# Kernel tuning notes

Measured on AMD Instinct MI355X. Metric: run time of the kernel, lower is better.

The kernel has to match this reference:

```python
import jax, jax.numpy as jnp
import numpy as np

B, U, C, M = 4096, 1024, 5000, 20

def setup_inputs() -> dict:
    key = jax.random.key(0)
    ks = jax.random.split(key, 9)
    inputs = jax.random.randint(ks[0], (B, 1), 0, C).astype(jnp.int32)
    states = 0.1 * jax.random.normal(ks[1], (B, U + 2), dtype=jnp.float32)
    bias_z = jnp.zeros((U,), jnp.float32)
    recurrent_kernel = 0.02 * jax.random.normal(ks[2], (U, 4 * U), dtype=jnp.float32)
    kernel_c = 0.02 * jax.random.normal(ks[3], (C, 4 * U), dtype=jnp.float32)
    bias = jnp.zeros((3 * U,), jnp.float32)
    kernel_d = 0.1 * jax.random.normal(ks[4], (2, 4 * U), dtype=jnp.float32)
    Wgmm_part1 = 0.05 * jax.random.normal(ks[5], (U, 3 * M), dtype=jnp.float32)
    bgmm_part1 = jnp.zeros((3 * M,), jnp.float32)
    return {"inputs": inputs, "states": states, "bias_z": bias_z,
            "recurrent_kernel": recurrent_kernel, "kernel_c": kernel_c,
            "bias": bias, "kernel_d": kernel_d,
            "Wgmm_part1": Wgmm_part1, "bgmm_part1": bgmm_part1}

def exp_safe(x):
    return jnp.clip(jnp.exp(x), 1e-10, 1e10)

def reference(inputs, states, bias_z, recurrent_kernel, kernel_c, bias,
              kernel_d, Wgmm_part1, bgmm_part1):
    u = bias_z.shape[0]
    h_tm1 = states[:, :-2]          # [B, U]
    _d = states[:, -2:]             # [B, 2]
    ch = inputs[:, 0].astype(jnp.int32)
    # one_hot(ch) @ kernel_c is just a row gather
    pre = kernel_c[ch] + _d @ kernel_d              # [B, 4U]
    # z and r gates share the left operand -> fuse into one matmul
    zr = (h_tm1 @ recurrent_kernel[:, :2 * u] + pre[:, :2 * u]
          + jnp.concatenate([bias_z, bias[:u]]))
    z = jax.nn.sigmoid(zr[:, :u])
    r = jax.nn.sigmoid(zr[:, u:])
    hh = jnp.tanh((r * h_tm1) @ recurrent_kernel[:, 2 * u:3 * u]
                  + pre[:, 2 * u:3 * u] + bias[u:2 * u])
    h = z * h_tm1 + (1.0 - z) * hh
    o = jnp.tanh(h @ recurrent_kernel[:, 3 * u:]
                 + pre[:, 3 * u:] + bias[2 * u:])
    gmm = o @ Wgmm_part1 + bgmm_part1               # [B, 3M]
    _pi, mux, muy = jnp.split(gmm, 3, axis=-1)
    e = exp_safe(_pi)
    pi = e / jnp.sum(e, axis=-1, keepdims=True)
    x_pred = jnp.sum(pi * mux, axis=-1, keepdims=True)
    y_pred = jnp.sum(pi * muy, axis=-1, keepdims=True)
    out = jnp.concatenate([o, pi, mux, muy, x_pred, y_pred], axis=-1)
    new_state = jnp.concatenate([h, x_pred, y_pred], axis=-1)
    return out, new_state
```

## Files before the change

### kernel.cpp

```cpp
#include <hip/hip_runtime.h>

typedef __attribute__((ext_vector_type(8))) short     bf16x8;
typedef __attribute__((ext_vector_type(4))) float     f32x4;
typedef __attribute__((ext_vector_type(2))) float     f32x2;
typedef __attribute__((ext_vector_type(4))) unsigned short u16x4;

#define OUT_STRIDE 1086
#define NS_STRIDE 1026
#define NS_BASE (4096*1086)

__device__ __forceinline__ unsigned short f2bf(float x) {
  unsigned int u = __float_as_uint(x);
  unsigned int r = (u + 0x7FFFu + ((u >> 16) & 1u)) >> 16;
  return (unsigned short)r;
}
__device__ __forceinline__ float bf2f(unsigned short u) {
  union { unsigned int i; float f; } v; v.i = ((unsigned int)u) << 16; return v.f;
}
__device__ __forceinline__ float sigmoidf(float x) { return 1.f / (1.f + expf(-x)); }

__device__ __forceinline__ void gld_lds16(const void* g, void* l) {
  __builtin_amdgcn_global_load_lds((const __attribute__((address_space(1))) void*)g,
                                   (__attribute__((address_space(3))) void*)l, 16, 0, 0);
}

__device__ __forceinline__ void decode_block(int bid, int& m0, int& n0) {
  const int swz = (bid & 7) * 64 + (bid >> 3);
  const int chunk = swz >> 6, l = swz & 63;
  m0 = ((chunk & 3) * 8 + (l >> 3)) * 128;
  n0 = ((chunk >> 2) * 8 + (l & 7)) * 64;
}

__global__ __launch_bounds__(256)
void transposeR(const float* __restrict__ R, unsigned short* __restrict__ Bt) {
  __shared__ float t[64][65];
  const int tx = threadIdx.x & 63, ty = threadIdx.x >> 6;
  const int j0 = blockIdx.x * 64, k0 = blockIdx.y * 64;
#pragma unroll
  for (int i = 0; i < 64; i += 4)
    t[ty + i][tx] = R[(size_t)(k0 + ty + i) * 4096 + j0 + tx];
  __syncthreads();
#pragma unroll
  for (int i = 0; i < 64; i += 4) {
    const int j = ty + i;
    Bt[(size_t)(j0 + j) * 1024 + k0 + tx] = f2bf(t[tx][j]);
  }
}

__global__ __launch_bounds__(256)
void convertH(const float* __restrict__ states, unsigned short* __restrict__ hb) {
  const int idx = blockIdx.x * 256 + threadIdx.x;
  const int b = idx >> 8, u = (idx & 255) * 4;
  const float* sp = states + (size_t)b * 1026 + u;
  f32x2 v0 = *(const f32x2*)sp, v1 = *(const f32x2*)(sp + 2);
  u16x4 w;
  w[0] = f2bf(v0[0]); w[1] = f2bf(v0[1]); w[2] = f2bf(v1[0]); w[3] = f2bf(v1[1]);
  *(u16x4*)&hb[(size_t)b * 1024 + u] = w;
}

__global__ __launch_bounds__(256)
void gemm_zr(const unsigned short* __restrict__ A,
             const unsigned short* __restrict__ Bt,
             const int* __restrict__ chv,
             const float* __restrict__ states,
             const float* __restrict__ kc,
             const float* __restrict__ kd,
             const float* __restrict__ bias_z,
             const float* __restrict__ bias,
             float* __restrict__ zbuf,
             unsigned short* __restrict__ rh) {
  __shared__ unsigned short Al[2][128 * 32];
  __shared__ unsigned short Bzl[2][64 * 32];
  __shared__ unsigned short Brl[2][64 * 32];
  __shared__ int   chs[128];
  __shared__ float d0s[128], d1s[128];

  const int tid = threadIdx.x, lane = tid & 63, wave = tid >> 6;
  int m0, n0;
  decode_block(blockIdx.x, m0, n0);

  if (tid < 128) {
    const int r = m0 + tid;
    chs[tid] = chv[r];
    d0s[tid] = states[(size_t)r * 1026 + 1024];
    d1s[tid] = states[(size_t)r * 1026 + 1025];
  }

  const unsigned short* Ag  = A  + (size_t)m0 * 1024;
  const unsigned short* Bzg = Bt + (size_t)n0 * 1024;
  const unsigned short* Brg = Bt + (size_t)(1024 + n0) * 1024;

  const int c1 = tid + 256;
  const int ar0 = tid >> 2, ak0 = (tid & 3) * 8;
  const int ar1 = c1 >> 2,  ak1 = (c1 & 3) * 8;

  f32x4 accz[2][4] = {}, accr[2][4] = {};

#define STAGE_ZR(b, kk)                                                        \
  gld_lds16(Ag  + (size_t)ar0 * 1024 + (kk) + ak0, &Al[b][tid * 8]);           \
  gld_lds16(Ag  + (size_t)ar1 * 1024 + (kk) + ak1, &Al[b][c1 * 8]);            \
  gld_lds16(Bzg + (size_t)ar0 * 1024 + (kk) + ak0, &Bzl[b][tid * 8]);          \
  gld_lds16(Brg + (size_t)ar0 * 1024 + (kk) + ak0, &Brl[b][tid * 8]);

  STAGE_ZR(0, 0);
  __syncthreads();

  const int arow = lane & 15, kg = (lane >> 4) * 8;
  for (int t = 0; t < 32; ++t) {
    const int cb = t & 1;
    if (t < 31) { STAGE_ZR(cb ^ 1, (t + 1) * 32); }
    bf16x8 af[2], bzf[4], brf[4];
#pragma unroll
    for (int mi = 0; mi < 2; ++mi)
      af[mi] = *(const bf16x8*)&Al[cb][(wave * 32 + mi * 16 + arow) * 32 + kg];
#pragma unroll
    for (int ni = 0; ni < 4; ++ni) {
      bzf[ni] = *(const bf16x8*)&Bzl[cb][(ni * 16 + arow) * 32 + kg];
      brf[ni] = *(const bf16x8*)&Brl[cb][(ni * 16 + arow) * 32 + kg];
    }
#pragma unroll
    for (int mi = 0; mi < 2; ++mi)
#pragma unroll
      for (int ni = 0; ni < 4; ++ni) {
        accz[mi][ni] = __builtin_amdgcn_mfma_f32_16x16x32_bf16(af[mi], bzf[ni], accz[mi][ni], 0, 0, 0);
        accr[mi][ni] = __builtin_amdgcn_mfma_f32_16x16x32_bf16(af[mi], brf[ni], accr[mi][ni], 0, 0, 0);
      }
    if (t < 31) __syncthreads();
  }
#undef STAGE_ZR

#pragma unroll
  for (int mi = 0; mi < 2; ++mi) {
#pragma unroll
    for (int r = 0; r < 4; ++r) {
      const int lrow = wave * 32 + mi * 16 + (lane >> 4) * 4 + r;
      const int grow = m0 + lrow;
      const int ch = chs[lrow];
      const float d0 = d0s[lrow], d1 = d1s[lrow];
      const float* kcrow = kc + (size_t)ch * 4096;
#pragma unroll
      for (int ni = 0; ni < 4; ++ni) {
        const int jc = n0 + ni * 16 + (lane & 15);
        const float vz = accz[mi][ni][r] + kcrow[jc]
                       + d0 * kd[jc] + d1 * kd[4096 + jc] + bias_z[jc];
        const float vr = accr[mi][ni][r] + kcrow[1024 + jc]
                       + d0 * kd[1024 + jc] + d1 * kd[4096 + 1024 + jc] + bias[jc];
        const float z = sigmoidf(vz);
        const float rr = sigmoidf(vr);
        zbuf[(size_t)grow * 1024 + jc] = z;
        rh[(size_t)grow * 1024 + jc] = f2bf(rr * bf2f(A[(size_t)grow * 1024 + jc]));
      }
    }
  }
}

template<int EPI>
__global__ __launch_bounds__(256)
void gemm_k(const unsigned short* __restrict__ A,
            const unsigned short* __restrict__ Bt,
            const int* __restrict__ chv,
            const float* __restrict__ states,
            const float* __restrict__ kc, int colbase,
            const float* __restrict__ kd,
            const float* __restrict__ bias, int biasoff,
            const float* __restrict__ zbuf,
            float* __restrict__ out2,
            unsigned short* __restrict__ hb2) {
  __shared__ unsigned short Al[2][128 * 32];
  __shared__ unsigned short Bl[2][64 * 32];
  __shared__ int   chs[128];
  __shared__ float d0s[128], d1s[128];

  const int tid = threadIdx.x, lane = tid & 63, wave = tid >> 6;
  int m0, n0;
  decode_block(blockIdx.x, m0, n0);

  if (tid < 128) {
    const int r = m0 + tid;
    chs[tid] = chv[r];
    d0s[tid] = states[(size_t)r * 1026 + 1024];
    d1s[tid] = states[(size_t)r * 1026 + 1025];
  }

  const unsigned short* Ag = A  + (size_t)m0 * 1024;
  const unsigned short* Bg = Bt + (size_t)n0 * 1024;

  const int c1 = tid + 256;
  const int ar0 = tid >> 2, ak0 = (tid & 3) * 8;
  const int ar1 = c1 >> 2,  ak1 = (c1 & 3) * 8;

  f32x4 acc[2][4] = {};

#define STAGE_K(b, kk)                                                         \
  gld_lds16(Ag + (size_t)ar0 * 1024 + (kk) + ak0, &Al[b][tid * 8]);            \
  gld_lds16(Ag + (size_t)ar1 * 1024 + (kk) + ak1, &Al[b][c1 * 8]);             \
  gld_lds16(Bg + (size_t)ar0 * 1024 + (kk) + ak0, &Bl[b][tid * 8]);

  STAGE_K(0, 0);
  __syncthreads();

  const int arow = lane & 15, kg = (lane >> 4) * 8;
  for (int t = 0; t < 32; ++t) {
    const int cb = t & 1;
    if (t < 31) { STAGE_K(cb ^ 1, (t + 1) * 32); }
    bf16x8 af[2], bf[4];
#pragma unroll
    for (int mi = 0; mi < 2; ++mi)
      af[mi] = *(const bf16x8*)&Al[cb][(wave * 32 + mi * 16 + arow) * 32 + kg];
#pragma unroll
    for (int ni = 0; ni < 4; ++ni)
      bf[ni] = *(const bf16x8*)&Bl[cb][(ni * 16 + arow) * 32 + kg];
#pragma unroll
    for (int mi = 0; mi < 2; ++mi)
#pragma unroll
      for (int ni = 0; ni < 4; ++ni)
        acc[mi][ni] = __builtin_amdgcn_mfma_f32_16x16x32_bf16(af[mi], bf[ni], acc[mi][ni], 0, 0, 0);
    if (t < 31) __syncthreads();
  }
#undef STAGE_K

#pragma unroll
  for (int mi = 0; mi < 2; ++mi) {
#pragma unroll
    for (int r = 0; r < 4; ++r) {
      const int lrow = wave * 32 + mi * 16 + (lane >> 4) * 4 + r;
      const int grow = m0 + lrow;
      const int ch = chs[lrow];
      const float d0 = d0s[lrow], d1 = d1s[lrow];
      const float* kcrow = kc + (size_t)ch * 4096 + colbase;
#pragma unroll
      for (int ni = 0; ni < 4; ++ni) {
        const int gcol = n0 + ni * 16 + (lane & 15);
        float v = acc[mi][ni][r] + kcrow[gcol]
                + d0 * kd[colbase + gcol] + d1 * kd[4096 + colbase + gcol]
                + bias[biasoff + gcol];
        if (EPI == 2) {
          const float hh = tanhf(v);
          const float z = zbuf[(size_t)grow * 1024 + gcol];
          const float htm = states[(size_t)grow * 1026 + gcol];
          const float h = z * htm + (1.f - z) * hh;
          out2[(size_t)grow * NS_STRIDE + gcol] = h;
          hb2[(size_t)grow * 1024 + gcol] = f2bf(h);
        } else {
          out2[(size_t)grow * OUT_STRIDE + gcol] = tanhf(v);
        }
      }
    }
  }
}

__global__ __launch_bounds__(512)
void gmm_kernel(const float* __restrict__ obuf,
                const float* __restrict__ Wg,
                const float* __restrict__ bg,
                float* __restrict__ outp,
                float* __restrict__ ns) {
  __shared__ float Wl[128 * 60 + 16];
  __shared__ float ol[8 * 1024];
  const int tid = threadIdx.x;
  const int lane = tid & 63;
  const int wave = tid >> 6;
  const int row0 = blockIdx.x * 8;

  for (int i = tid; i < 4096; i += 512) {
    const int rr = i >> 9, c2 = (i & 511) * 2;
    *(f32x2*)&ol[rr * 1024 + c2] = *(const f32x2*)&obuf[(size_t)(row0 + rr) * OUT_STRIDE + c2];
  }

  float g = 0.f;
  for (int kc0 = 0; kc0 < 1024; kc0 += 128) {
    __syncthreads();
    for (int i = tid; i < 1920; i += 512)
      *(f32x4*)&Wl[i * 4] = *(const f32x4*)&Wg[kc0 * 60 + i * 4];
    __syncthreads();
    const float* orow = &ol[wave * 1024 + kc0];
#pragma unroll 8
    for (int k = 0; k < 128; ++k)
      g = fmaf(orow[k], Wl[k * 60 + lane], g);
  }
  if (lane < 60) g += bg[lane];

  float e = 0.f;
  if (lane < 20) e = fminf(fmaxf(expf(g), 1e-10f), 1e10f);
  float s = e;
#pragma unroll
  for (int m = 1; m < 32; m <<= 1) s += __shfl_xor(s, m, 64);
  const float pi = (lane < 20) ? e / s : 0.f;
  const int src1 = (lane < 20) ? lane + 20 : lane;
  const int src2 = (lane < 20) ? lane + 40 : lane;
  const float mux = __shfl(g, src1, 64);
  const float muy = __shfl(g, src2, 64);
  float px = pi * mux, py = pi * muy;
#pragma unroll
  for (int m = 1; m < 32; m <<= 1) { px += __shfl_xor(px, m, 64); py += __shfl_xor(py, m, 64); }

  const int row = row0 + wave;
  float* orow = outp + (size_t)row * OUT_STRIDE;
  if (lane < 20) orow[1024 + lane] = pi;
  else if (lane < 60) orow[1024 + lane] = g;
  if (lane == 0) {
    orow[1084] = px;
    orow[1085] = py;
    ns[(size_t)row * NS_STRIDE + 1024] = px;
    ns[(size_t)row * NS_STRIDE + 1025] = py;
  }
}

extern "C" void kernel_launch(void* const* d_in, const int* in_sizes, int n_in,
                              void* d_out, int out_size, void* d_ws, size_t ws_size,
                              hipStream_t stream) {
  const int*   chv    = (const int*)d_in[0];
  const float* states = (const float*)d_in[1];
  const float* bias_z = (const float*)d_in[2];
  const float* R      = (const float*)d_in[3];
  const float* kc     = (const float*)d_in[4];
  const float* bias   = (const float*)d_in[5];
  const float* kd     = (const float*)d_in[6];
  const float* Wg     = (const float*)d_in[7];
  const float* bg     = (const float*)d_in[8];
  float* out = (float*)d_out;

  char* ws = (char*)d_ws;
  unsigned short* RbT  = (unsigned short*)ws;
  unsigned short* hb   = (unsigned short*)(ws + 8388608);
  unsigned short* rh   = (unsigned short*)(ws + 16777216);
  unsigned short* hb2  = (unsigned short*)(ws + 25165824);
  float*          zbuf = (float*)(ws + 33554432);

  transposeR<<<dim3(64, 16), 256, 0, stream>>>(R, RbT);
  convertH<<<4096, 256, 0, stream>>>(states, hb);

  gemm_zr<<<512, 256, 0, stream>>>(hb, RbT, chv, states, kc, kd, bias_z, bias, zbuf, rh);

  gemm_k<2><<<512, 256, 0, stream>>>(rh, RbT + (size_t)2048 * 1024,
      chv, states, kc, 2048, kd, bias, 1024, zbuf, out + NS_BASE, hb2);

  gemm_k<3><<<512, 256, 0, stream>>>(hb2, RbT + (size_t)3072 * 1024,
      chv, states, kc, 3072, kd, bias, 2048, nullptr, out, nullptr);

  gmm_kernel<<<512, 512, 0, stream>>>(out, Wg, bg, out, out + NS_BASE);
}
```

Baseline: 339.8 us.

## Deepen GEMM K-loop pipeline to 4 LDS buffers with vmcnt-based waits

Both GEMM kernels move from a double-buffered LDS pipeline to a 4-slot ring with two stages in flight. They replace __syncthreads with explicit s_waitcnt vmcnt counts plus s_barrier, so a wave waits only for the stage it is about to consume. They also raise wave priority around the MFMA block with s_setprio. The aim is to hide global-load latency better, at the cost of doubled LDS use (lower occupancy) and fragile hand-counted vmcnt values. There is no barrier protecting a slot from being overwritten while a slower wave still reads it, which depends on the 4-slot distance.

```diff
diff --git a/kernel.cpp b/kernel.cpp
--- a/kernel.cpp
+++ b/kernel.cpp
@@ -69,9 +69,9 @@
              const float* __restrict__ bias,
              float* __restrict__ zbuf,
              unsigned short* __restrict__ rh) {
-  __shared__ unsigned short Al[2][128 * 32];
-  __shared__ unsigned short Bzl[2][64 * 32];
-  __shared__ unsigned short Brl[2][64 * 32];
+  __shared__ unsigned short Al[4][128 * 32];
+  __shared__ unsigned short Bzl[4][64 * 32];
+  __shared__ unsigned short Brl[4][64 * 32];
   __shared__ int   chs[128];
   __shared__ float d0s[128], d1s[128];
 
@@ -95,6 +95,7 @@
   const int ar1 = c1 >> 2,  ak1 = (c1 & 3) * 8;
 
   f32x4 accz[2][4] = {}, accr[2][4] = {};
+  const int arow = lane & 15, kg = (lane >> 4) * 8;
 
 #define STAGE_ZR(b, kk)                                                        \
   gld_lds16(Ag  + (size_t)ar0 * 1024 + (kk) + ak0, &Al[b][tid * 8]);           \
@@ -102,13 +103,7 @@
   gld_lds16(Bzg + (size_t)ar0 * 1024 + (kk) + ak0, &Bzl[b][tid * 8]);          \
   gld_lds16(Brg + (size_t)ar0 * 1024 + (kk) + ak0, &Brl[b][tid * 8]);
 
-  STAGE_ZR(0, 0);
-  __syncthreads();
-
-  const int arow = lane & 15, kg = (lane >> 4) * 8;
-  for (int t = 0; t < 32; ++t) {
-    const int cb = t & 1;
-    if (t < 31) { STAGE_ZR(cb ^ 1, (t + 1) * 32); }
+  auto compute = [&](int cb) {
     bf16x8 af[2], bzf[4], brf[4];
 #pragma unroll
     for (int mi = 0; mi < 2; ++mi)
@@ -118,6 +113,7 @@
       bzf[ni] = *(const bf16x8*)&Bzl[cb][(ni * 16 + arow) * 32 + kg];
       brf[ni] = *(const bf16x8*)&Brl[cb][(ni * 16 + arow) * 32 + kg];
     }
+    __builtin_amdgcn_s_setprio(1);
 #pragma unroll
     for (int mi = 0; mi < 2; ++mi)
 #pragma unroll
@@ -125,8 +121,27 @@
         accz[mi][ni] = __builtin_amdgcn_mfma_f32_16x16x32_bf16(af[mi], bzf[ni], accz[mi][ni], 0, 0, 0);
         accr[mi][ni] = __builtin_amdgcn_mfma_f32_16x16x32_bf16(af[mi], brf[ni], accr[mi][ni], 0, 0, 0);
       }
-    if (t < 31) __syncthreads();
-  }
+    __builtin_amdgcn_s_setprio(0);
+  };
+
+  STAGE_ZR(0, 0);
+  STAGE_ZR(1, 32);
+  for (int t = 0; t < 30; ++t) {
+    const int nx = (t + 2) & 3;
+    STAGE_ZR(nx, (t + 2) * 32);
+    asm volatile("s_waitcnt vmcnt(8)" ::: "memory");
+    __builtin_amdgcn_s_barrier();
+    asm volatile("" ::: "memory");
+    compute(t & 3);
+  }
+  asm volatile("s_waitcnt vmcnt(4)" ::: "memory");
+  __builtin_amdgcn_s_barrier();
+  asm volatile("" ::: "memory");
+  compute(2);
+  asm volatile("s_waitcnt vmcnt(0)" ::: "memory");
+  __builtin_amdgcn_s_barrier();
+  asm volatile("" ::: "memory");
+  compute(3);
 #undef STAGE_ZR
 
 #pragma unroll
@@ -166,8 +181,8 @@
             const float* __restrict__ zbuf,
             float* __restrict__ out2,
             unsigned short* __restrict__ hb2) {
-  __shared__ unsigned short Al[2][128 * 32];
-  __shared__ unsigned short Bl[2][64 * 32];
+  __shared__ unsigned short Al[4][128 * 32];
+  __shared__ unsigned short Bl[4][64 * 32];
   __shared__ int   chs[128];
   __shared__ float d0s[128], d1s[128];
 
@@ -190,33 +205,48 @@
   const int ar1 = c1 >> 2,  ak1 = (c1 & 3) * 8;
 
   f32x4 acc[2][4] = {};
+  const int arow = lane & 15, kg = (lane >> 4) * 8;
 
 #define STAGE_K(b, kk)                                                         \
   gld_lds16(Ag + (size_t)ar0 * 1024 + (kk) + ak0, &Al[b][tid * 8]);            \
   gld_lds16(Ag + (size_t)ar1 * 1024 + (kk) + ak1, &Al[b][c1 * 8]);             \
   gld_lds16(Bg + (size_t)ar0 * 1024 + (kk) + ak0, &Bl[b][tid * 8]);
 
-  STAGE_K(0, 0);
-  __syncthreads();
-
-  const int arow = lane & 15, kg = (lane >> 4) * 8;
-  for (int t = 0; t < 32; ++t) {
-    const int cb = t & 1;
-    if (t < 31) { STAGE_K(cb ^ 1, (t + 1) * 32); }
-    bf16x8 af[2], bf[4];
+  auto compute = [&](int cb) {
+    bf16x8 af[2], bfr[4];
 #pragma unroll
     for (int mi = 0; mi < 2; ++mi)
       af[mi] = *(const bf16x8*)&Al[cb][(wave * 32 + mi * 16 + arow) * 32 + kg];
 #pragma unroll
     for (int ni = 0; ni < 4; ++ni)
-      bf[ni] = *(const bf16x8*)&Bl[cb][(ni * 16 + arow) * 32 + kg];
+      bfr[ni] = *(const bf16x8*)&Bl[cb][(ni * 16 + arow) * 32 + kg];
+    __builtin_amdgcn_s_setprio(1);
 #pragma unroll
     for (int mi = 0; mi < 2; ++mi)
 #pragma unroll
       for (int ni = 0; ni < 4; ++ni)
-        acc[mi][ni] = __builtin_amdgcn_mfma_f32_16x16x32_bf16(af[mi], bf[ni], acc[mi][ni], 0, 0, 0);
-    if (t < 31) __syncthreads();
-  }
+        acc[mi][ni] = __builtin_amdgcn_mfma_f32_16x16x32_bf16(af[mi], bfr[ni], acc[mi][ni], 0, 0, 0);
+    __builtin_amdgcn_s_setprio(0);
+  };
+
+  STAGE_K(0, 0);
+  STAGE_K(1, 32);
+  for (int t = 0; t < 30; ++t) {
+    const int nx = (t + 2) & 3;
+    STAGE_K(nx, (t + 2) * 32);
+    asm volatile("s_waitcnt vmcnt(6)" ::: "memory");
+    __builtin_amdgcn_s_barrier();
+    asm volatile("" ::: "memory");
+    compute(t & 3);
+  }
+  asm volatile("s_waitcnt vmcnt(3)" ::: "memory");
+  __builtin_amdgcn_s_barrier();
+  asm volatile("" ::: "memory");
+  compute(2);
+  asm volatile("s_waitcnt vmcnt(0)" ::: "memory");
+  __builtin_amdgcn_s_barrier();
+  asm volatile("" ::: "memory");
+  compute(3);
 #undef STAGE_K
 
 #pragma unroll
```

Measured after the change: 328.7 us. 1.03x faster.
